# Optimization experiments

Hardware: AMD Instinct MI355X
Metric: run time of the kernel (lower is better)

Reference implementation:

```python
import jax, jax.numpy as jnp
import numpy as np

B = 16384
TEXT_D = 768
TECH_D = 256
IN_D = TEXT_D + TECH_D  # 1024
OUT_D = 1024
E = 8


def setup_inputs() -> dict:
    key = jax.random.key(0)
    ks = jax.random.split(key, 8)
    s_in = 1.0 / np.sqrt(IN_D)
    s_out = 1.0 / np.sqrt(OUT_D)
    return {
        "text_features": jax.random.normal(ks[0], (B, TEXT_D), jnp.float32),
        "technical_features": jax.random.normal(ks[1], (B, TECH_D), jnp.float32),
        # stacked expert params: layer1 [E, IN_D, OUT_D], layer2 [E, OUT_D, OUT_D]
        "W1": jax.random.uniform(ks[2], (E, IN_D, OUT_D), jnp.float32, -s_in, s_in),
        "b1": jax.random.uniform(ks[3], (E, OUT_D), jnp.float32, -s_in, s_in),
        "W2": jax.random.uniform(ks[4], (E, OUT_D, OUT_D), jnp.float32, -s_out, s_out),
        "b2": jax.random.uniform(ks[5], (E, OUT_D), jnp.float32, -s_out, s_out),
        # gating network
        "Wg": jax.random.uniform(ks[6], (IN_D, E), jnp.float32, -s_in, s_in),
        "bg": jax.random.uniform(ks[7], (E,), jnp.float32, -s_in, s_in),
    }


def reference(text_features, technical_features, W1, b1, W2, b2, Wg, bg):
    x = jnp.concatenate([text_features, technical_features], axis=-1)  # [B, IN_D]
    gates = jax.nn.softmax(x @ Wg + bg, axis=-1)                       # [B, E]
    h = jax.nn.relu(jnp.einsum('bi,eio->beo', x, W1) + b1[None])       # [B, E, OUT_D]
    y = jnp.einsum('beo,eop->bep', h, W2) + b2[None]                   # [B, E, OUT_D]
    return jnp.einsum('be,bep->bp', gates, y)                          # [B, OUT_D]
```

## Files before the change

kernel.cpp:

```cpp
#include <hip/hip_runtime.h>
#include <hip/hip_bf16.h>

#define NB 16384
#define TEXT_D 768
#define TECH_D 256
#define IND 1024
#define OUTD 1024
#define NE 8
#define KH2 4096

typedef unsigned short u16;
typedef __bf16 bf16x8 __attribute__((ext_vector_type(8)));
typedef float f32x4 __attribute__((ext_vector_type(4)));

__device__ __forceinline__ u16 f2bf(float f) {
  union { float f; unsigned int u; } x; x.f = f;
  unsigned int u = x.u;
  return (u16)((u + 0x7FFFu + ((u >> 16) & 1u)) >> 16);
}

__device__ __forceinline__ void gload_lds16(const void* g, void* l) {
  __builtin_amdgcn_global_load_lds(
      (const __attribute__((address_space(1))) unsigned int*)g,
      (__attribute__((address_space(3))) unsigned int*)l, 16, 0, 0);
}

__global__ __launch_bounds__(256) void convert_gates(
    const float* __restrict__ text, const float* __restrict__ tech,
    const float* __restrict__ Wg, const float* __restrict__ bg,
    u16* __restrict__ xb, float* __restrict__ gates) {
  int t = threadIdx.x;
  int wave = t >> 6, lane = t & 63;
  int row = blockIdx.x * 4 + wave;

  float acc[NE];
#pragma unroll
  for (int e = 0; e < NE; ++e) acc[e] = 0.f;

#pragma unroll
  for (int j = 0; j < 4; ++j) {
    int col = j * 256 + lane * 4;
    float4 v = (j < 3) ? *(const float4*)&text[(size_t)row * TEXT_D + col]
                       : *(const float4*)&tech[(size_t)row * TECH_D + lane * 4];
    ushort4 o = make_ushort4(f2bf(v.x), f2bf(v.y), f2bf(v.z), f2bf(v.w));
    *(ushort4*)&xb[(size_t)row * IND + col] = o;
    const float* wp = &Wg[(size_t)col * NE];
    float xv[4] = {v.x, v.y, v.z, v.w};
#pragma unroll
    for (int i = 0; i < 4; ++i) {
      float4 w0 = *(const float4*)&wp[i * NE];
      float4 w1 = *(const float4*)&wp[i * NE + 4];
      acc[0] = fmaf(xv[i], w0.x, acc[0]);
      acc[1] = fmaf(xv[i], w0.y, acc[1]);
      acc[2] = fmaf(xv[i], w0.z, acc[2]);
      acc[3] = fmaf(xv[i], w0.w, acc[3]);
      acc[4] = fmaf(xv[i], w1.x, acc[4]);
      acc[5] = fmaf(xv[i], w1.y, acc[5]);
      acc[6] = fmaf(xv[i], w1.z, acc[6]);
      acc[7] = fmaf(xv[i], w1.w, acc[7]);
    }
  }
#pragma unroll
  for (int off = 32; off; off >>= 1)
#pragma unroll
    for (int e = 0; e < NE; ++e) acc[e] += __shfl_xor(acc[e], off);

#pragma unroll
  for (int e = 0; e < NE; ++e) acc[e] += bg[e];
  float mx = acc[0];
#pragma unroll
  for (int e = 1; e < NE; ++e) mx = fmaxf(mx, acc[e]);
  float s = 0.f;
#pragma unroll
  for (int e = 0; e < NE; ++e) { acc[e] = expf(acc[e] - mx); s += acc[e]; }
  float inv = 1.f / s;
  if (lane < NE) gates[(size_t)row * NE + lane] = acc[lane] * inv;
}

__global__ __launch_bounds__(256) void transpose_w12(
    const float* __restrict__ W1, const float* __restrict__ W2,
    u16* __restrict__ W1t, u16* __restrict__ W2t) {
  __shared__ u16 tile[64][65];
  int bid = blockIdx.x;
  int half = bid >> 11;
  int b2 = bid & 2047;
  int e = b2 >> 8;
  int tb = b2 & 255;
  int r0 = (tb >> 4) * 64;
  int c0 = (tb & 15) * 64;
  const float* We; u16* Wte; int ostride;
  if (half == 0) {
    We = W1 + (size_t)e * IND * OUTD;
    Wte = W1t + ((size_t)e << 20);
    ostride = 1024;
  } else {
    We = W2 + (size_t)e * IND * OUTD;
    Wte = W2t + ((size_t)(e >> 2) << 22) + (size_t)(e & 3) * 1024;
    ostride = KH2;
  }
  int t = threadIdx.x;
  int tr = t >> 4;
  int tc = (t & 15) * 4;
#pragma unroll
  for (int j = 0; j < 4; ++j) {
    int row = j * 16 + tr;
    float4 v = *(const float4*)&We[(size_t)(r0 + row) * OUTD + c0 + tc];
    tile[row][tc + 0] = f2bf(v.x);
    tile[row][tc + 1] = f2bf(v.y);
    tile[row][tc + 2] = f2bf(v.z);
    tile[row][tc + 3] = f2bf(v.w);
  }
  __syncthreads();
#pragma unroll
  for (int j = 0; j < 4; ++j) {
    int row = j * 16 + tr;
    ushort4 o = make_ushort4(tile[tc + 0][row], tile[tc + 1][row],
                             tile[tc + 2][row], tile[tc + 3][row]);
    *(ushort4*)&Wte[(size_t)(c0 + row) * ostride + r0 + tc] = o;
  }
}

#define BAR() asm volatile("s_barrier" ::: "memory")
#define VM0() asm volatile("s_waitcnt vmcnt(0)" ::: "memory")
#define VM4() asm volatile("s_waitcnt vmcnt(4)" ::: "memory")
#define LG0()                                            \
  do {                                                   \
    asm volatile("s_waitcnt lgkmcnt(0)" ::: "memory");   \
    __builtin_amdgcn_sched_barrier(0);                   \
  } while (0)

template <int SLOT, int K>
__device__ __forceinline__ void stage_slot(
    const u16* __restrict__ pA, const u16* __restrict__ pB, char* sb, int k0,
    int ch0, int rsub, int koff, int lbyte) {
#pragma unroll
  for (int j = 0; j < 2; ++j) {
    int ch = ch0 + j;
    int r;
    if constexpr (SLOT == 0)      r = (ch >> 3) * 128 + (ch & 7) * 8 + rsub;
    else if constexpr (SLOT == 3) r = 64 + (ch >> 3) * 128 + (ch & 7) * 8 + rsub;
    else if constexpr (SLOT == 1) r = (ch >> 2) * 64 + (ch & 3) * 8 + rsub;
    else                          r = (ch >> 2) * 64 + 32 + (ch & 3) * 8 + rsub;
    const u16* g = (SLOT == 0 || SLOT == 3) ? pA : pB;
    char* lb = sb + ((SLOT == 0 || SLOT == 3) ? 0 : 32768) + r * 128 + lbyte;
    gload_lds16(g + (size_t)r * K + k0 + koff, lb);
  }
}

template <int QH>
__device__ __forceinline__ void load_a(const char* rb, int wr, int lr, int hi,
                                       int swr, bf16x8 (&a)[4][2]) {
#pragma unroll
  for (int i = 0; i < 4; ++i)
#pragma unroll
    for (int ks = 0; ks < 2; ++ks)
      a[i][ks] = *(const bf16x8*)(rb + (wr * 128 + QH * 64 + i * 16 + lr) * 128
                                  + ((ks * 64 + hi * 16) ^ swr));
}

template <int NH>
__device__ __forceinline__ void load_b(const char* rb, int wc, int lr, int hi,
                                       int swr, bf16x8 (&b)[2][2]) {
#pragma unroll
  for (int q = 0; q < 2; ++q)
#pragma unroll
    for (int ks = 0; ks < 2; ++ks)
      b[q][ks] = *(const bf16x8*)(rb + 32768 +
                                  (wc * 64 + (NH * 2 + q) * 16 + lr) * 128
                                  + ((ks * 64 + hi * 16) ^ swr));
}

template <int MH, int NH>
__device__ __forceinline__ void mfma_quad(const bf16x8 (&a)[4][2],
                                          const bf16x8 (&b)[2][2],
                                          f32x4 (&acc)[8][4]) {
  __builtin_amdgcn_s_setprio(1);
#pragma unroll
  for (int i = 0; i < 4; ++i)
#pragma unroll
    for (int q = 0; q < 2; ++q) {
      acc[MH*4+i][NH*2+q] = __builtin_amdgcn_mfma_f32_16x16x32_bf16(
          a[i][0], b[q][0], acc[MH*4+i][NH*2+q], 0, 0, 0);
      acc[MH*4+i][NH*2+q] = __builtin_amdgcn_mfma_f32_16x16x32_bf16(
          a[i][1], b[q][1], acc[MH*4+i][NH*2+q], 0, 0, 0);
    }
  __builtin_amdgcn_s_setprio(0);
}

template <int RB, int K, bool LAST>
__device__ __forceinline__ void ktile(
    const u16* __restrict__ pA, const u16* __restrict__ pB, char* lds,
    int kNext, int ch0, int rsub, int koff, int lbyte,
    int wr, int wc, int lr, int hi, int swr,
    bf16x8 (&a)[4][2], bf16x8 (&b0)[2][2], bf16x8 (&b1)[2][2],
    f32x4 (&acc)[8][4]) {
  const char* rb = lds + RB * 65536;
  char* sb = lds + (RB ^ 1) * 65536;
  load_a<0>(rb, wr, lr, hi, swr, a);
  load_b<0>(rb, wc, lr, hi, swr, b0);
  if constexpr (!LAST) {
    stage_slot<0, K>(pA, pB, sb, kNext, ch0, rsub, koff, lbyte);
    stage_slot<1, K>(pA, pB, sb, kNext, ch0, rsub, koff, lbyte);
  }
  BAR(); LG0();
  mfma_quad<0, 0>(a, b0, acc);
  if constexpr (LAST) { VM0(); } else { VM4(); }
  BAR();
  load_b<1>(rb, wc, lr, hi, swr, b1);
  if constexpr (!LAST) {
    stage_slot<2, K>(pA, pB, sb, kNext, ch0, rsub, koff, lbyte);
    stage_slot<3, K>(pA, pB, sb, kNext, ch0, rsub, koff, lbyte);
  }
  BAR(); LG0();
  mfma_quad<0, 1>(a, b1, acc);
  BAR();
  load_a<1>(rb, wr, lr, hi, swr, a);
  BAR(); LG0();
  mfma_quad<1, 0>(a, b0, acc);
  BAR();
  mfma_quad<1, 1>(a, b1, acc);
  if constexpr (!LAST) { VM4(); }
  BAR();
}

template <int K>
__device__ __forceinline__ void core256(const u16* __restrict__ pA,
                                        const u16* __restrict__ pB,
                                        char* lds, int t, f32x4 (&acc)[8][4]) {
  constexpr int KT = K / 64;
  static_assert(KT >= 4 && (KT & 1) == 0, "KT must be even >= 4");
  const int l = t & 63;
  const int w = t >> 6;
  const int wr = w >> 2, wc = w & 3;
  const int lr = l & 15, hi = l >> 4;
  const int rsub = l >> 3;
  const int koff = ((l & 7) ^ rsub) << 3;
  const int lbyte = (l & 7) * 16;
  const int ch0 = w * 2;
  const int swr = (lr & 7) << 4;

  bf16x8 a[4][2], b0[2][2], b1[2][2];

  stage_slot<0, K>(pA, pB, lds, 0, ch0, rsub, koff, lbyte);
  stage_slot<1, K>(pA, pB, lds, 0, ch0, rsub, koff, lbyte);
  stage_slot<2, K>(pA, pB, lds, 0, ch0, rsub, koff, lbyte);
  stage_slot<3, K>(pA, pB, lds, 0, ch0, rsub, koff, lbyte);
  VM4(); BAR();

  for (int T = 0; T < KT - 2; T += 2) {
    ktile<0, K, false>(pA, pB, lds, (T + 1) * 64, ch0, rsub, koff, lbyte,
                       wr, wc, lr, hi, swr, a, b0, b1, acc);
    ktile<1, K, false>(pA, pB, lds, (T + 2) * 64, ch0, rsub, koff, lbyte,
                       wr, wc, lr, hi, swr, a, b0, b1, acc);
  }
  ktile<0, K, false>(pA, pB, lds, (KT - 1) * 64, ch0, rsub, koff, lbyte,
                     wr, wc, lr, hi, swr, a, b0, b1, acc);
  ktile<1, K, true>(pA, pB, lds, 0, ch0, rsub, koff, lbyte,
                    wr, wc, lr, hi, swr, a, b0, b1, acc);
}

__global__ __launch_bounds__(512, 2) void gemm1(
    const u16* __restrict__ xb, const u16* __restrict__ W1t,
    const float* __restrict__ b1, const float* __restrict__ gates,
    u16* __restrict__ Hg, int eg0) {
  __shared__ char lds[131072];
  int t = threadIdx.x;
  int nwg = gridDim.x, cpx = nwg >> 3, bid = blockIdx.x;
  int swz = (bid & 7) * cpx + (bid >> 3);
  int nb = swz & 3, ee = (swz >> 2) & 3, mb = swz >> 4;
  int e = eg0 + ee;

  f32x4 acc[8][4] = {};
  core256<1024>(xb + (size_t)mb * 256 * 1024,
                W1t + ((size_t)e << 20) + (size_t)nb * 256 * 1024,
                lds, t, acc);

  int l = t & 63, w = t >> 6, wr = w >> 2, wc = w & 3, lr = l & 15, hi = l >> 4;
  int m0 = mb * 256 + wr * 128 + hi * 4;
  int n0 = nb * 256 + wc * 64 + lr;
  const float* b1e = b1 + e * OUTD;
#pragma unroll
  for (int m = 0; m < 8; ++m) {
#pragma unroll
    for (int r = 0; r < 4; ++r) {
      int row = m0 + m * 16 + r;
      float g = gates[(size_t)row * NE + e];
#pragma unroll
      for (int nn = 0; nn < 4; ++nn) {
        int n = n0 + nn * 16;
        float v = g * fmaxf(acc[m][nn][r] + b1e[n], 0.f);
        Hg[(size_t)row * KH2 + ee * 1024 + n] = f2bf(v);
      }
    }
  }
}

template <bool FIRST>
__global__ __launch_bounds__(512, 2) void gemm2(
    const u16* __restrict__ Hg, const u16* __restrict__ W2th,
    const float* __restrict__ b2h, const float* __restrict__ gates,
    float* __restrict__ out, int eg0) {
  __shared__ char lds[131072];
  int t = threadIdx.x;
  int nwg = gridDim.x, cpx = nwg >> 3, bid = blockIdx.x;
  int swz = (bid & 7) * cpx + (bid >> 3);
  int nb = swz & 3, mb = swz >> 2;

  f32x4 acc[8][4] = {};
  core256<KH2>(Hg + (size_t)mb * 256 * KH2, W2th + (size_t)nb * 256 * KH2,
               lds, t, acc);

  int l = t & 63, w = t >> 6, wr = w >> 2, wc = w & 3, lr = l & 15, hi = l >> 4;
  int m0 = mb * 256 + wr * 128 + hi * 4;
  int n0 = nb * 256 + wc * 64 + lr;

  float bcol[4][4];
#pragma unroll
  for (int nn = 0; nn < 4; ++nn)
#pragma unroll
    for (int j = 0; j < 4; ++j)
      bcol[nn][j] = b2h[j * OUTD + n0 + nn * 16];

#pragma unroll
  for (int m = 0; m < 8; ++m) {
#pragma unroll
    for (int r = 0; r < 4; ++r) {
      int row = m0 + m * 16 + r;
      float4 ga = *(const float4*)&gates[(size_t)row * NE + eg0];
#pragma unroll
      for (int nn = 0; nn < 4; ++nn) {
        float bias = ga.x * bcol[nn][0] + ga.y * bcol[nn][1] +
                     ga.z * bcol[nn][2] + ga.w * bcol[nn][3];
        size_t oi = (size_t)row * OUTD + n0 + nn * 16;
        float v = acc[m][nn][r] + bias;
        if (FIRST) out[oi] = v;
        else       out[oi] += v;
      }
    }
  }
}

extern "C" void kernel_launch(void* const* d_in, const int* in_sizes, int n_in,
                              void* d_out, int out_size, void* d_ws, size_t ws_size,
                              hipStream_t stream) {
  (void)in_sizes; (void)n_in; (void)out_size; (void)ws_size;
  const float* text = (const float*)d_in[0];
  const float* tech = (const float*)d_in[1];
  const float* W1   = (const float*)d_in[2];
  const float* b1   = (const float*)d_in[3];
  const float* W2   = (const float*)d_in[4];
  const float* b2   = (const float*)d_in[5];
  const float* Wg   = (const float*)d_in[6];
  const float* bg   = (const float*)d_in[7];
  float* out = (float*)d_out;

  char* p = (char*)d_ws;
  u16* xb  = (u16*)p;  p += (size_t)NB * IND * 2;
  u16* W1t = (u16*)p;  p += (size_t)NE * IND * OUTD * 2;
  u16* W2t = (u16*)p;  p += (size_t)NE * OUTD * OUTD * 2;
  float* gates = (float*)p; p += (size_t)NB * NE * 4;
  u16* Hg  = (u16*)p;

  convert_gates<<<dim3(NB / 4), dim3(256), 0, stream>>>(text, tech, Wg, bg, xb, gates);
  transpose_w12<<<dim3(4096), dim3(256), 0, stream>>>(W1, W2, W1t, W2t);

  for (int h = 0; h < 2; ++h) {
    int eg0 = h * 4;
    gemm1<<<dim3(1024), dim3(512), 0, stream>>>(xb, W1t, b1, gates, Hg, eg0);
    const u16* W2th = W2t + ((size_t)h << 22);
    const float* b2h = b2 + (size_t)eg0 * OUTD;
    if (h == 0)
      gemm2<true><<<dim3(256), dim3(512), 0, stream>>>(Hg, W2th, b2h, gates, out, eg0);
    else
      gemm2<false><<<dim3(256), dim3(512), 0, stream>>>(Hg, W2th, b2h, gates, out, eg0);
  }
}
```

Measured before the change: 623.1 us.

## Prefetch next k-tile LDS fragments and rebalance global-to-LDS staging waits

Restructures the per-k-tile schedule so the A and B register fragments for the next tile are read from LDS at the end of the current tile, letting the first MFMA quad start with no LDS wait. Global-to-LDS stage slots are regrouped (three before the first barrier, one after), with vmcnt waits changed from 4 to 6 and 2. The MFMA loop order is also changed to iterate over k-substeps outermost, spacing out dependent accumulations. The risks are tighter ordering between the LDS buffer swap and the vmcnt waits, and extra register pressure from holding the prefetched fragments.

```diff
diff --git a/kernel.cpp b/kernel.cpp
--- a/kernel.cpp
+++ b/kernel.cpp
@@ -122,7 +122,8 @@
 
 #define BAR() asm volatile("s_barrier" ::: "memory")
 #define VM0() asm volatile("s_waitcnt vmcnt(0)" ::: "memory")
-#define VM4() asm volatile("s_waitcnt vmcnt(4)" ::: "memory")
+#define VM2() asm volatile("s_waitcnt vmcnt(2)" ::: "memory")
+#define VM6() asm volatile("s_waitcnt vmcnt(6)" ::: "memory")
 #define LG0()                                            \
   do {                                                   \
     asm volatile("s_waitcnt lgkmcnt(0)" ::: "memory");   \
@@ -176,14 +177,13 @@
                                           f32x4 (&acc)[8][4]) {
   __builtin_amdgcn_s_setprio(1);
 #pragma unroll
-  for (int i = 0; i < 4; ++i)
-#pragma unroll
-    for (int q = 0; q < 2; ++q) {
-      acc[MH*4+i][NH*2+q] = __builtin_amdgcn_mfma_f32_16x16x32_bf16(
-          a[i][0], b[q][0], acc[MH*4+i][NH*2+q], 0, 0, 0);
-      acc[MH*4+i][NH*2+q] = __builtin_amdgcn_mfma_f32_16x16x32_bf16(
-          a[i][1], b[q][1], acc[MH*4+i][NH*2+q], 0, 0, 0);
-    }
+  for (int ks = 0; ks < 2; ++ks)
+#pragma unroll
+    for (int i = 0; i < 4; ++i)
+#pragma unroll
+      for (int q = 0; q < 2; ++q)
+        acc[MH*4+i][NH*2+q] = __builtin_amdgcn_mfma_f32_16x16x32_bf16(
+            a[i][ks], b[q][ks], acc[MH*4+i][NH*2+q], 0, 0, 0);
   __builtin_amdgcn_s_setprio(0);
 }
 
@@ -196,30 +196,32 @@
     f32x4 (&acc)[8][4]) {
   const char* rb = lds + RB * 65536;
   char* sb = lds + (RB ^ 1) * 65536;
-  load_a<0>(rb, wr, lr, hi, swr, a);
-  load_b<0>(rb, wc, lr, hi, swr, b0);
+  LG0();
+  mfma_quad<0, 0>(a, b0, acc);
   if constexpr (!LAST) {
     stage_slot<0, K>(pA, pB, sb, kNext, ch0, rsub, koff, lbyte);
     stage_slot<1, K>(pA, pB, sb, kNext, ch0, rsub, koff, lbyte);
-  }
-  BAR(); LG0();
-  mfma_quad<0, 0>(a, b0, acc);
-  if constexpr (LAST) { VM0(); } else { VM4(); }
+    stage_slot<2, K>(pA, pB, sb, kNext, ch0, rsub, koff, lbyte);
+  }
+  load_b<1>(rb, wc, lr, hi, swr, b1);
+  if constexpr (!LAST) { VM6(); }
+  else                 { VM0(); }
   BAR();
-  load_b<1>(rb, wc, lr, hi, swr, b1);
-  if constexpr (!LAST) {
-    stage_slot<2, K>(pA, pB, sb, kNext, ch0, rsub, koff, lbyte);
+  LG0();
+  mfma_quad<0, 1>(a, b1, acc);
+  if constexpr (!LAST)
     stage_slot<3, K>(pA, pB, sb, kNext, ch0, rsub, koff, lbyte);
-  }
-  BAR(); LG0();
-  mfma_quad<0, 1>(a, b1, acc);
+  load_a<1>(rb, wr, lr, hi, swr, a);
   BAR();
-  load_a<1>(rb, wr, lr, hi, swr, a);
-  BAR(); LG0();
+  LG0();
   mfma_quad<1, 0>(a, b0, acc);
+  if constexpr (!LAST) { VM2(); }
   BAR();
   mfma_quad<1, 1>(a, b1, acc);
-  if constexpr (!LAST) { VM4(); }
+  if constexpr (!LAST) {
+    load_a<0>(sb, wr, lr, hi, swr, a);
+    load_b<0>(sb, wc, lr, hi, swr, b0);
+  }
   BAR();
 }
 
@@ -245,7 +247,9 @@
   stage_slot<1, K>(pA, pB, lds, 0, ch0, rsub, koff, lbyte);
   stage_slot<2, K>(pA, pB, lds, 0, ch0, rsub, koff, lbyte);
   stage_slot<3, K>(pA, pB, lds, 0, ch0, rsub, koff, lbyte);
-  VM4(); BAR();
+  VM0(); BAR();
+  load_a<0>(lds, wr, lr, hi, swr, a);
+  load_b<0>(lds, wc, lr, hi, swr, b0);
 
   for (int T = 0; T < KT - 2; T += 2) {
     ktile<0, K, false>(pA, pB, lds, (T + 1) * 64, ch0, rsub, koff, lbyte,
```

New measurement: 690.0 us. 1.11x slower.
